# Kernel optimization log

Hardware: AMD Instinct MI355X
Metric: run time of the kernel (lower is better)

## Reference

```python
import jax, jax.numpy as jnp
import numpy as np

N = 50000   # nodes
E = 800000  # edges (avg degree 16)
D = 128     # feature dim (indim = outdim)
EPS = 1e-6


def setup_inputs() -> dict:
    key = jax.random.key(0)
    ks = jax.random.split(key, 13)
    s = 1.0 / np.sqrt(D)
    inp = {
        "h": jax.random.normal(ks[0], (N, D), jnp.float32),
        "e": jax.random.normal(ks[1], (E, D), jnp.float32),
        "norm": jax.random.uniform(ks[2], (N, 1), jnp.float32),
        "src": jax.random.randint(ks[3], (E,), 0, N),
        "dst": jax.random.randint(ks[4], (E,), 0, N),
        # four single-layer projections A, B, D, E (n_mlp_layer=1, activation=None)
        "WA": jax.random.normal(ks[5], (D, D), jnp.float32) * s,
        "bA": jax.random.normal(ks[6], (D,), jnp.float32) * 0.01,
        "WB": jax.random.normal(ks[7], (D, D), jnp.float32) * s,
        "bB": jax.random.normal(ks[8], (D,), jnp.float32) * 0.01,
        "WD": jax.random.normal(ks[9], (D, D), jnp.float32) * s,
        "bD": jax.random.normal(ks[10], (D,), jnp.float32) * 0.01,
        "WE": jax.random.normal(ks[11], (D, D), jnp.float32) * s,
        "bE": jax.random.normal(ks[12], (D,), jnp.float32) * 0.01,
    }
    return inp


def reference(h, e, norm, src, dst, WA, bA, WB, bB, WD, bD, WE, bE):
    # h = h * norm  (symmetric degree normalization)
    hn = h * norm
    # four linear projections on nodes
    Ah = hn @ WA + bA
    Bh = hn @ WB + bB
    Dh = hn @ WD + bD
    Eh = hn @ WE + bE
    # per-edge gate: e_ij = Dh[src] + Eh[dst]; sigma = sigmoid(e_ij)
    eg = Dh[src] + Eh[dst]            # [E, D]
    sigma = jax.nn.sigmoid(eg)        # [E, D]
    # weighted segment-sum aggregation onto destination nodes
    num = jax.ops.segment_sum(sigma * Bh[src], dst, num_segments=N)  # [N, D]
    den = jax.ops.segment_sum(sigma, dst, num_segments=N)            # [N, D]
    h_out = Ah + num / (den + EPS)
    # h = h * norm again (post-normalization); batch_norm off, residual off,
    # dropout(p=0) is identity
    h_out = h_out * norm
    return (h_out, e)
```

## Files before the change

kernel.cpp:

```cpp
#include <hip/hip_runtime.h>
#include <math.h>

#define DIM 128
#define CAP 128

__global__ __launch_bounds__(256) void proj4_kernel(
    const float* __restrict__ h, const float* __restrict__ norm,
    const float* __restrict__ W0, const float* __restrict__ b0,
    const float* __restrict__ W1, const float* __restrict__ b1,
    const float* __restrict__ W2, const float* __restrict__ b2,
    const float* __restrict__ W3, const float* __restrict__ b3,
    float* __restrict__ O0, float* __restrict__ O1,
    float* __restrict__ O2, float* __restrict__ O3, int N)
{
    __shared__ float sA[64][132];
    __shared__ float sW[32][132];

    const int tid = threadIdx.x;
    const int rowBase = blockIdx.x * 64;

    for (int i = tid; i < 64 * DIM; i += 256) {
        int r = i >> 7, c = i & 127;
        int gr = rowBase + r;
        float v = 0.0f;
        if (gr < N) v = h[(size_t)gr * DIM + c] * norm[gr];
        sA[r][c] = v;
    }

    const float* Ws[4] = {W0, W1, W2, W3};
    const float* bs[4] = {b0, b1, b2, b3};
    float* Os[4] = {O0, O1, O2, O3};

    const int c0 = (tid & 31) * 4;
    const int r0 = (tid >> 5) * 8;
    const int wrow = tid >> 3;
    const int wcol = (tid & 7) * 16;

    for (int p = 0; p < 4; ++p) {
        const float* W = Ws[p];

        float4 pre0, pre1, pre2, pre3;
        {
            const float* Wp = W + (size_t)wrow * DIM + wcol;
            pre0 = *(const float4*)&Wp[0];
            pre1 = *(const float4*)&Wp[4];
            pre2 = *(const float4*)&Wp[8];
            pre3 = *(const float4*)&Wp[12];
        }

        float acc[8][4];
        #pragma unroll
        for (int i = 0; i < 8; ++i) {
            #pragma unroll
            for (int j = 0; j < 4; ++j) acc[i][j] = 0.0f;
        }

        for (int kc = 0; kc < DIM; kc += 32) {
            __syncthreads();
            *(float4*)&sW[wrow][wcol]      = pre0;
            *(float4*)&sW[wrow][wcol + 4]  = pre1;
            *(float4*)&sW[wrow][wcol + 8]  = pre2;
            *(float4*)&sW[wrow][wcol + 12] = pre3;
            __syncthreads();

            if (kc + 32 < DIM) {
                const float* Wp = W + (size_t)(kc + 32 + wrow) * DIM + wcol;
                pre0 = *(const float4*)&Wp[0];
                pre1 = *(const float4*)&Wp[4];
                pre2 = *(const float4*)&Wp[8];
                pre3 = *(const float4*)&Wp[12];
            }

            #pragma unroll 4
            for (int k = 0; k < 32; k += 4) {
                float4 w[4];
                #pragma unroll
                for (int kk = 0; kk < 4; ++kk)
                    w[kk] = *(const float4*)&sW[k + kk][c0];
                #pragma unroll
                for (int i = 0; i < 8; ++i) {
                    float4 a = *(const float4*)&sA[r0 + i][kc + k];
                    acc[i][0] += a.x * w[0].x; acc[i][1] += a.x * w[0].y;
                    acc[i][2] += a.x * w[0].z; acc[i][3] += a.x * w[0].w;
                    acc[i][0] += a.y * w[1].x; acc[i][1] += a.y * w[1].y;
                    acc[i][2] += a.y * w[1].z; acc[i][3] += a.y * w[1].w;
                    acc[i][0] += a.z * w[2].x; acc[i][1] += a.z * w[2].y;
                    acc[i][2] += a.z * w[2].z; acc[i][3] += a.z * w[2].w;
                    acc[i][0] += a.w * w[3].x; acc[i][1] += a.w * w[3].y;
                    acc[i][2] += a.w * w[3].z; acc[i][3] += a.w * w[3].w;
                }
            }
        }

        float4 bias = *(const float4*)&bs[p][c0];
        float* O = Os[p];
        #pragma unroll
        for (int i = 0; i < 8; ++i) {
            int gr = rowBase + r0 + i;
            if (gr < N) {
                float4 o;
                o.x = acc[i][0] + bias.x;
                o.y = acc[i][1] + bias.y;
                o.z = acc[i][2] + bias.z;
                o.w = acc[i][3] + bias.w;
                *(float4*)&O[(size_t)gr * DIM + c0] = o;
            }
        }
    }
}

__global__ void count_fill_kernel(const int* __restrict__ src,
                                  const int* __restrict__ dst,
                                  int* __restrict__ cnt,
                                  int* __restrict__ csr, int E)
{
    int e = blockIdx.x * blockDim.x + threadIdx.x;
    if (e < E) {
        int d = dst[e];
        int pos = atomicAdd(&cnt[d], 1);
        if (pos < CAP) csr[(size_t)d * CAP + pos] = src[e];
    }
}

__global__ __launch_bounds__(256) void aggregate_kernel(
    const float* __restrict__ Ah, const float* __restrict__ Bh,
    const float* __restrict__ Dh, const float* __restrict__ Eh,
    const float* __restrict__ norm,
    const int* __restrict__ cnt, const int* __restrict__ csr,
    float* __restrict__ out, int N)
{
    const int lane = threadIdx.x & 63;
    const int wv   = threadIdx.x >> 6;
    const int n    = blockIdx.x * 4 + wv;
    if (n >= N) return;

    const int half = lane >> 5;
    const int c0   = (lane & 31) * 4;

    int deg = cnt[n];
    if (deg > CAP) deg = CAP;

    const float4 eh = *(const float4*)&Eh[(size_t)n * DIM + c0];
    const int* crow = csr + (size_t)n * CAP;

    float nx = 0.f, ny = 0.f, nz = 0.f, nw = 0.f;
    float dx = 0.f, dy = 0.f, dz = 0.f, dw = 0.f;

    #pragma unroll 2
    for (int j = 0; j < deg; j += 2) {
        int jj = j + half;
        bool act = jj < deg;
        int s = crow[act ? jj : j];
        float4 dv = *(const float4*)&Dh[(size_t)s * DIM + c0];
        float4 bv = *(const float4*)&Bh[(size_t)s * DIM + c0];
        float sx = 1.0f / (1.0f + __expf(-(dv.x + eh.x)));
        float sy = 1.0f / (1.0f + __expf(-(dv.y + eh.y)));
        float sz = 1.0f / (1.0f + __expf(-(dv.z + eh.z)));
        float sw = 1.0f / (1.0f + __expf(-(dv.w + eh.w)));
        if (!act) { sx = 0.f; sy = 0.f; sz = 0.f; sw = 0.f; }
        nx += sx * bv.x; ny += sy * bv.y; nz += sz * bv.z; nw += sw * bv.w;
        dx += sx; dy += sy; dz += sz; dw += sw;
    }

    nx += __shfl_xor(nx, 32); ny += __shfl_xor(ny, 32);
    nz += __shfl_xor(nz, 32); nw += __shfl_xor(nw, 32);
    dx += __shfl_xor(dx, 32); dy += __shfl_xor(dy, 32);
    dz += __shfl_xor(dz, 32); dw += __shfl_xor(dw, 32);

    if (half == 0) {
        float4 av = *(const float4*)&Ah[(size_t)n * DIM + c0];
        float nm = norm[n];
        float4 o;
        o.x = (av.x + nx / (dx + 1e-6f)) * nm;
        o.y = (av.y + ny / (dy + 1e-6f)) * nm;
        o.z = (av.z + nz / (dz + 1e-6f)) * nm;
        o.w = (av.w + nw / (dw + 1e-6f)) * nm;
        *(float4*)&out[(size_t)n * DIM + c0] = o;
    }
}

__global__ void copy_e_kernel(const float4* __restrict__ in,
                              float4* __restrict__ out, int n4)
{
    int i = blockIdx.x * blockDim.x + threadIdx.x;
    int stride = gridDim.x * blockDim.x;
    for (; i < n4; i += stride) out[i] = in[i];
}

extern "C" void kernel_launch(void* const* d_in, const int* in_sizes, int n_in,
                              void* d_out, int out_size, void* d_ws, size_t ws_size,
                              hipStream_t stream)
{
    const float* h    = (const float*)d_in[0];
    const float* e    = (const float*)d_in[1];
    const float* norm = (const float*)d_in[2];
    const int*   src  = (const int*)d_in[3];
    const int*   dst  = (const int*)d_in[4];
    const float* WA = (const float*)d_in[5];
    const float* bA = (const float*)d_in[6];
    const float* WB = (const float*)d_in[7];
    const float* bB = (const float*)d_in[8];
    const float* WD = (const float*)d_in[9];
    const float* bD = (const float*)d_in[10];
    const float* WE = (const float*)d_in[11];
    const float* bE = (const float*)d_in[12];

    const int N = in_sizes[0] / DIM;
    const int E = in_sizes[3];

    float* out_h = (float*)d_out;
    float* out_e = out_h + (size_t)N * DIM;

    float* ws = (float*)d_ws;
    float* Ah = ws;
    float* Bh = Ah + (size_t)N * DIM;
    float* Dh = Bh + (size_t)N * DIM;
    float* Eh = Dh + (size_t)N * DIM;
    int* cnt  = (int*)(Eh + (size_t)N * DIM);
    int* csr  = cnt + N;

    hipMemsetAsync(cnt, 0, (size_t)N * sizeof(int), stream);

    count_fill_kernel<<<(E + 255) / 256, 256, 0, stream>>>(src, dst, cnt, csr, E);

    proj4_kernel<<<(N + 63) / 64, 256, 0, stream>>>(
        h, norm, WA, bA, WB, bB, WD, bD, WE, bE, Ah, Bh, Dh, Eh, N);

    aggregate_kernel<<<(N + 3) / 4, 256, 0, stream>>>(
        Ah, Bh, Dh, Eh, norm, cnt, csr, out_h, N);

    const int n4 = (E * DIM) / 4;
    copy_e_kernel<<<4096, 256, 0, stream>>>((const float4*)e, (float4*)out_e, n4);
}
```

Measured before the change: 997.1 us.

## Fuse edge-feature passthrough copy into projection and aggregation kernels

Removes the standalone copy kernel for the edge tensor. The 400 MB copy is split so that the projection GEMM kernel streams one chunk per k-step and the aggregation kernel copies the rest with nontemporal loads and stores. This hides copy bandwidth behind compute- and latency-bound work. In exchange it adds register pressure and extra memory traffic inside both kernels, and the gather loop unroll rises from 2 to 4.

New measurement: 929.6 us. 6.8% less time.

```diff
diff --git a/kernel.cpp b/kernel.cpp
--- a/kernel.cpp
+++ b/kernel.cpp
@@ -3,6 +3,8 @@
 
 #define DIM 128
 #define CAP 128
+
+typedef float __attribute__((ext_vector_type(4))) f4v;
 
 __global__ __launch_bounds__(256) void proj4_kernel(
     const float* __restrict__ h, const float* __restrict__ norm,
@@ -11,7 +13,8 @@
     const float* __restrict__ W2, const float* __restrict__ b2,
     const float* __restrict__ W3, const float* __restrict__ b3,
     float* __restrict__ O0, float* __restrict__ O1,
-    float* __restrict__ O2, float* __restrict__ O3, int N)
+    float* __restrict__ O2, float* __restrict__ O3, int N,
+    const f4v* __restrict__ e_in, f4v* __restrict__ e_out)
 {
     __shared__ float sA[64][132];
     __shared__ float sW[32][132];
@@ -35,6 +38,8 @@
     const int r0 = (tid >> 5) * 8;
     const int wrow = tid >> 3;
     const int wcol = (tid & 7) * 16;
+
+    int t = 0;
 
     for (int p = 0; p < 4; ++p) {
         const float* W = Ws[p];
@@ -70,6 +75,10 @@
                 pre2 = *(const float4*)&Wp[8];
                 pre3 = *(const float4*)&Wp[12];
             }
+
+            const size_t cb = ((size_t)t * gridDim.x + blockIdx.x) * 512 + tid;
+            f4v cv0 = __builtin_nontemporal_load(e_in + cb);
+            f4v cv1 = __builtin_nontemporal_load(e_in + cb + 256);
 
             #pragma unroll 4
             for (int k = 0; k < 32; k += 4) {
@@ -90,6 +99,10 @@
                     acc[i][2] += a.w * w[3].z; acc[i][3] += a.w * w[3].w;
                 }
             }
+
+            __builtin_nontemporal_store(cv0, e_out + cb);
+            __builtin_nontemporal_store(cv1, e_out + cb + 256);
+            ++t;
         }
 
         float4 bias = *(const float4*)&bs[p][c0];
@@ -127,64 +140,81 @@
     const float* __restrict__ Dh, const float* __restrict__ Eh,
     const float* __restrict__ norm,
     const int* __restrict__ cnt, const int* __restrict__ csr,
-    float* __restrict__ out, int N)
-{
+    float* __restrict__ out, int N,
+    const f4v* __restrict__ e_in, f4v* __restrict__ e_out,
+    int copyBase, int n4)
+{
+    const size_t cb = (size_t)copyBase + (size_t)blockIdx.x * 1536 + threadIdx.x;
+    f4v c0v, c1v, c2v, c3v, c4v, c5v;
+    const bool g0 = cb            < (size_t)n4;
+    const bool g1 = cb + 256      < (size_t)n4;
+    const bool g2 = cb + 512      < (size_t)n4;
+    const bool g3 = cb + 768      < (size_t)n4;
+    const bool g4 = cb + 1024     < (size_t)n4;
+    const bool g5 = cb + 1280     < (size_t)n4;
+    if (g0) c0v = __builtin_nontemporal_load(e_in + cb);
+    if (g1) c1v = __builtin_nontemporal_load(e_in + cb + 256);
+    if (g2) c2v = __builtin_nontemporal_load(e_in + cb + 512);
+    if (g3) c3v = __builtin_nontemporal_load(e_in + cb + 768);
+    if (g4) c4v = __builtin_nontemporal_load(e_in + cb + 1024);
+    if (g5) c5v = __builtin_nontemporal_load(e_in + cb + 1280);
+
     const int lane = threadIdx.x & 63;
     const int wv   = threadIdx.x >> 6;
     const int n    = blockIdx.x * 4 + wv;
-    if (n >= N) return;
-
-    const int half = lane >> 5;
-    const int c0   = (lane & 31) * 4;
-
-    int deg = cnt[n];
-    if (deg > CAP) deg = CAP;
-
-    const float4 eh = *(const float4*)&Eh[(size_t)n * DIM + c0];
-    const int* crow = csr + (size_t)n * CAP;
-
-    float nx = 0.f, ny = 0.f, nz = 0.f, nw = 0.f;
-    float dx = 0.f, dy = 0.f, dz = 0.f, dw = 0.f;
-
-    #pragma unroll 2
-    for (int j = 0; j < deg; j += 2) {
-        int jj = j + half;
-        bool act = jj < deg;
-        int s = crow[act ? jj : j];
-        float4 dv = *(const float4*)&Dh[(size_t)s * DIM + c0];
-        float4 bv = *(const float4*)&Bh[(size_t)s * DIM + c0];
-        float sx = 1.0f / (1.0f + __expf(-(dv.x + eh.x)));
-        float sy = 1.0f / (1.0f + __expf(-(dv.y + eh.y)));
-        float sz = 1.0f / (1.0f + __expf(-(dv.z + eh.z)));
-        float sw = 1.0f / (1.0f + __expf(-(dv.w + eh.w)));
-        if (!act) { sx = 0.f; sy = 0.f; sz = 0.f; sw = 0.f; }
-        nx += sx * bv.x; ny += sy * bv.y; nz += sz * bv.z; nw += sw * bv.w;
-        dx += sx; dy += sy; dz += sz; dw += sw;
-    }
-
-    nx += __shfl_xor(nx, 32); ny += __shfl_xor(ny, 32);
-    nz += __shfl_xor(nz, 32); nw += __shfl_xor(nw, 32);
-    dx += __shfl_xor(dx, 32); dy += __shfl_xor(dy, 32);
-    dz += __shfl_xor(dz, 32); dw += __shfl_xor(dw, 32);
-
-    if (half == 0) {
-        float4 av = *(const float4*)&Ah[(size_t)n * DIM + c0];
-        float nm = norm[n];
-        float4 o;
-        o.x = (av.x + nx / (dx + 1e-6f)) * nm;
-        o.y = (av.y + ny / (dy + 1e-6f)) * nm;
-        o.z = (av.z + nz / (dz + 1e-6f)) * nm;
-        o.w = (av.w + nw / (dw + 1e-6f)) * nm;
-        *(float4*)&out[(size_t)n * DIM + c0] = o;
-    }
-}
-
-__global__ void copy_e_kernel(const float4* __restrict__ in,
-                              float4* __restrict__ out, int n4)
-{
-    int i = blockIdx.x * blockDim.x + threadIdx.x;
-    int stride = gridDim.x * blockDim.x;
-    for (; i < n4; i += stride) out[i] = in[i];
+
+    if (n < N) {
+        const int half = lane >> 5;
+        const int c0   = (lane & 31) * 4;
+
+        int deg = cnt[n];
+        if (deg > CAP) deg = CAP;
+
+        const float4 eh = *(const float4*)&Eh[(size_t)n * DIM + c0];
+        const int* crow = csr + (size_t)n * CAP;
+
+        float nx = 0.f, ny = 0.f, nz = 0.f, nw = 0.f;
+        float dx = 0.f, dy = 0.f, dz = 0.f, dw = 0.f;
+
+        #pragma unroll 4
+        for (int j = 0; j < deg; j += 2) {
+            int jj = j + half;
+            bool act = jj < deg;
+            int s = crow[act ? jj : j];
+            float4 dv = *(const float4*)&Dh[(size_t)s * DIM + c0];
+            float4 bv = *(const float4*)&Bh[(size_t)s * DIM + c0];
+            float sx = 1.0f / (1.0f + __expf(-(dv.x + eh.x)));
+            float sy = 1.0f / (1.0f + __expf(-(dv.y + eh.y)));
+            float sz = 1.0f / (1.0f + __expf(-(dv.z + eh.z)));
+            float sw = 1.0f / (1.0f + __expf(-(dv.w + eh.w)));
+            if (!act) { sx = 0.f; sy = 0.f; sz = 0.f; sw = 0.f; }
+            nx += sx * bv.x; ny += sy * bv.y; nz += sz * bv.z; nw += sw * bv.w;
+            dx += sx; dy += sy; dz += sz; dw += sw;
+        }
+
+        nx += __shfl_xor(nx, 32); ny += __shfl_xor(ny, 32);
+        nz += __shfl_xor(nz, 32); nw += __shfl_xor(nw, 32);
+        dx += __shfl_xor(dx, 32); dy += __shfl_xor(dy, 32);
+        dz += __shfl_xor(dz, 32); dw += __shfl_xor(dw, 32);
+
+        if (half == 0) {
+            float4 av = *(const float4*)&Ah[(size_t)n * DIM + c0];
+            float nm = norm[n];
+            float4 o;
+            o.x = (av.x + nx / (dx + 1e-6f)) * nm;
+            o.y = (av.y + ny / (dy + 1e-6f)) * nm;
+            o.z = (av.z + nz / (dz + 1e-6f)) * nm;
+            o.w = (av.w + nw / (dw + 1e-6f)) * nm;
+            *(float4*)&out[(size_t)n * DIM + c0] = o;
+        }
+    }
+
+    if (g0) __builtin_nontemporal_store(c0v, e_out + cb);
+    if (g1) __builtin_nontemporal_store(c1v, e_out + cb + 256);
+    if (g2) __builtin_nontemporal_store(c2v, e_out + cb + 512);
+    if (g3) __builtin_nontemporal_store(c3v, e_out + cb + 768);
+    if (g4) __builtin_nontemporal_store(c4v, e_out + cb + 1024);
+    if (g5) __builtin_nontemporal_store(c5v, e_out + cb + 1280);
 }
 
 extern "C" void kernel_launch(void* const* d_in, const int* in_sizes, int n_in,
@@ -223,12 +253,15 @@
 
     count_fill_kernel<<<(E + 255) / 256, 256, 0, stream>>>(src, dst, cnt, csr, E);
 
-    proj4_kernel<<<(N + 63) / 64, 256, 0, stream>>>(
-        h, norm, WA, bA, WB, bB, WD, bD, WE, bE, Ah, Bh, Dh, Eh, N);
+    const int n4 = (E * DIM) / 4;
+    const int gridP = (N + 63) / 64;
+    const int Q = gridP * 16 * 512;
+
+    proj4_kernel<<<gridP, 256, 0, stream>>>(
+        h, norm, WA, bA, WB, bB, WD, bD, WE, bE, Ah, Bh, Dh, Eh, N,
+        (const f4v*)e, (f4v*)out_e);
 
     aggregate_kernel<<<(N + 3) / 4, 256, 0, stream>>>(
-        Ah, Bh, Dh, Eh, norm, cnt, csr, out_h, N);
-
-    const int n4 = (E * DIM) / 4;
-    copy_e_kernel<<<4096, 256, 0, stream>>>((const float4*)e, (float4*)out_e, n4);
-}
+        Ah, Bh, Dh, Eh, norm, cnt, csr, out_h, N,
+        (const f4v*)e, (f4v*)out_e, Q, n4);
+}
```
